# Optimization experiments

Hardware: AMD Instinct MI355X
Metric: run time of the kernel (lower is better)

## Reference

```python
import jax, jax.numpy as jnp
import numpy as np
import math

H = 1024
NH = 16
D = H // NH  # 64
EPS = 1e-5


def _layernorm(x, g, b):
    mu = jnp.mean(x, axis=-1, keepdims=True)
    var = jnp.mean(jnp.square(x - mu), axis=-1, keepdims=True)
    return (x - mu) * jax.lax.rsqrt(var + EPS) * g + b


def setup_inputs() -> dict:
    key = jax.random.key(0)
    ks = jax.random.split(key, 12)
    B, T = 2, 2048
    q = jax.random.normal(ks[0], (B, T, H), jnp.float32)
    k = jax.random.normal(ks[1], (B, T, H), jnp.float32)
    v = jax.random.normal(ks[2], (B, T, H), jnp.float32)
    pad_mask = jax.random.randint(ks[3], (B, T), 0, 2) > 0
    s = 0.02
    Wq = jax.random.normal(ks[4], (H, H), jnp.float32) * s
    Wk = jax.random.normal(ks[5], (H, H), jnp.float32) * s
    Wv = jax.random.normal(ks[6], (H, H), jnp.float32) * s
    Wo = jax.random.normal(ks[7], (H, H), jnp.float32) * s
    W1 = jax.random.normal(ks[8], (4 * H, H), jnp.float32) * s
    b1 = jnp.zeros((4 * H,), jnp.float32)
    W2 = jax.random.normal(ks[9], (H, 4 * H), jnp.float32) * s
    b2 = jnp.zeros((H,), jnp.float32)
    g1 = jnp.ones((H,), jnp.float32); be1 = jnp.zeros((H,), jnp.float32)
    g2 = jnp.ones((H,), jnp.float32); be2 = jnp.zeros((H,), jnp.float32)
    return dict(q=q, k=k, v=v, pad_mask=pad_mask, Wq=Wq, Wk=Wk, Wv=Wv, Wo=Wo,
                W1=W1, b1=b1, W2=W2, b2=b2, g1=g1, be1=be1, g2=g2, be2=be2)


def reference(q, k, v, pad_mask, Wq, Wk, Wv, Wo, W1, b1, W2, b2, g1, be1, g2, be2):
    B, Tq, _ = q.shape
    Tv = v.shape[1]
    # torch nn.Linear: x @ W.T
    Q = (q @ Wq.T).reshape(B, NH, Tq, D)  # faithful to torch .view head split
    K = (k @ Wk.T).reshape(B, NH, Tv, D)
    V = (v @ Wv.T).reshape(B, NH, Tv, D)
    logits = jnp.einsum('baih,bajh->baij', Q, K)  # [B,NH,Tq,Tv]
    neg_inf = jnp.float32(-jnp.inf)
    logits = jnp.where(pad_mask[:, None, None, :], logits, neg_inf)
    attn = jax.nn.softmax(logits / math.sqrt(D), axis=-1)
    # post-softmax query-mask multiply (custom)
    attn = attn * pad_mask[:, None, :, None].astype(attn.dtype)
    h = jnp.einsum('baij,bajh->baih', attn, V).reshape(B, Tq, H)
    h = h @ Wo.T
    h = _layernorm(q + h, g1, be1)
    ff = jax.nn.gelu(h @ W1.T + b1, approximate=False) @ W2.T + b2  # dropout = identity (eval)
    return _layernorm(h + ff, g2, be2)
```

## Files before the change

### kernel.cpp

```cpp
#include <hip/hip_runtime.h>

typedef unsigned short u16;
typedef unsigned int u32;
typedef __attribute__((ext_vector_type(8))) __bf16 bf16x8;
typedef __attribute__((ext_vector_type(4))) float f32x4;
typedef __attribute__((ext_vector_type(16))) float f32x16;
typedef __attribute__((ext_vector_type(4))) unsigned short u16x4;
typedef __attribute__((ext_vector_type(8))) unsigned short u16x8;

#define LOG2E 1.44269504088896340736f

__device__ __forceinline__ u16 f2bf(float f) {
  union { float f; unsigned u; } c; c.f = f;
  unsigned r = c.u + 0x7FFFu + ((c.u >> 16) & 1u);
  return (u16)(r >> 16);
}
__device__ __forceinline__ float bf2f(u16 h) {
  union { unsigned u; float f; } c; c.u = ((unsigned)h) << 16;
  return c.f;
}

__device__ __forceinline__ void gload_lds16(const u16* g, u16* l) {
  __builtin_amdgcn_global_load_lds((const __attribute__((address_space(1))) unsigned int*)g,
                                   (__attribute__((address_space(3))) unsigned int*)l, 16, 0, 0);
}

__device__ __forceinline__ float gelu_fast(float x) {
  float z = fabsf(x) * 0.70710678118654752f;
  float t = 1.0f / (1.0f + 0.3275911f * z);
  float poly = t * (0.254829592f + t * (-0.284496736f + t * (1.421413741f +
               t * (-1.453152027f + t * 1.061405429f))));
  float e = __builtin_amdgcn_exp2f(-z * z * LOG2E);
  float erfz = 1.0f - poly * e;
  float s = (x >= 0.0f) ? erfz : -erfz;
  return 0.5f * x * (1.0f + s);
}

__global__ __launch_bounds__(256) void cvt_all(
    const float* __restrict__ s0, const float* __restrict__ s1, const float* __restrict__ s2,
    const float* __restrict__ s3, const float* __restrict__ s4, const float* __restrict__ s5,
    const float* __restrict__ s6, const float* __restrict__ s7, const float* __restrict__ s8,
    u16* __restrict__ d0, u16* __restrict__ d1, u16* __restrict__ d2,
    u16* __restrict__ d3, u16* __restrict__ d4, u16* __restrict__ d5,
    u16* __restrict__ d6, u16* __restrict__ d7, u16* __restrict__ d8) {
  int i = blockIdx.x * 256 + threadIdx.x;
  if (i >= 6291456) return;
  const float* src; u16* dst; int off;
  if (i < 3145728) {
    if (i < 1048576)      { src = s0; dst = d0; off = 0; }
    else if (i < 2097152) { src = s1; dst = d1; off = 1048576; }
    else                  { src = s2; dst = d2; off = 2097152; }
  } else if (i < 4194304) {
    if (i < 3407872)      { src = s3; dst = d3; off = 3145728; }
    else if (i < 3670016) { src = s4; dst = d4; off = 3407872; }
    else if (i < 3932160) { src = s5; dst = d5; off = 3670016; }
    else                  { src = s6; dst = d6; off = 3932160; }
  } else {
    if (i < 5242880)      { src = s7; dst = d7; off = 4194304; }
    else                  { src = s8; dst = d8; off = 5242880; }
  }
  int j = i - off;
  f32x4 v = ((const f32x4*)src)[j];
  u16x4 o;
  o[0] = f2bf(v[0]); o[1] = f2bf(v[1]); o[2] = f2bf(v[2]); o[3] = f2bf(v[3]);
  ((u16x4*)dst)[j] = o;
}

__global__ void build_masks(const void* __restrict__ pm, float* __restrict__ maskbias,
                            float* __restrict__ qmask, int n) {
  __shared__ int sflag;
  if (threadIdx.x == 0) sflag = 0;
  __syncthreads();
  const unsigned* pw = (const unsigned*)pm;
  int nwords = n / 4;
  int local = 0;
  for (int i = threadIdx.x; i < nwords; i += blockDim.x)
    if (pw[i] > 1u) local = 1;
  if (local) atomicOr(&sflag, 1);
  __syncthreads();
  bool isbool = (sflag != 0);
  for (int i = threadIdx.x; i < n; i += blockDim.x) {
    int m = isbool ? (int)((const unsigned char*)pm)[i] : ((const int*)pm)[i];
    maskbias[i] = m ? 0.0f : -2e30f;
    qmask[i]    = m ? 1.0f : 0.0f;
  }
}

template<int EPI>
__device__ __forceinline__ void gemm_core(const u16* __restrict__ A, const u16* __restrict__ Bw,
                                          const float* __restrict__ bias, u16* __restrict__ C,
                                          int N, int Kstride, int Klen, int bn, int bm, int tid) {
  __shared__ u16 smem[3][8192];
  int wave = tid >> 6, lane = tid & 63;
  int l15 = lane & 15, l4 = lane >> 4;
  int wr = (wave >> 1) * 64, wc = (wave & 1) * 64;
  int mrow0 = bm * 128, ncol0 = bn * 128;
  int srow = lane >> 2;
  int scol = (lane & 3) * 8;

  const u16* asrc0 = A  + (size_t)(mrow0 + (wave * 2 + 0) * 16 + srow) * Kstride + scol;
  const u16* asrc1 = A  + (size_t)(mrow0 + (wave * 2 + 1) * 16 + srow) * Kstride + scol;
  const u16* bsrc0 = Bw + (size_t)(ncol0 + (wave * 2 + 0) * 16 + srow) * Kstride + scol;
  const u16* bsrc1 = Bw + (size_t)(ncol0 + (wave * 2 + 1) * 16 + srow) * Kstride + scol;
  u16* ad0 = &smem[0][(wave * 2 + 0) * 512];
  u16* ad1 = &smem[0][(wave * 2 + 1) * 512];
  u16* bd0 = &smem[0][4096 + (wave * 2 + 0) * 512];
  u16* bd1 = &smem[0][4096 + (wave * 2 + 1) * 512];

  auto stage = [&](int buf, int k0) {
    gload_lds16(asrc0 + k0, ad0 + buf * 8192);
    gload_lds16(asrc1 + k0, ad1 + buf * 8192);
    gload_lds16(bsrc0 + k0, bd0 + buf * 8192);
    gload_lds16(bsrc1 + k0, bd1 + buf * 8192);
  };

  f32x4 acc[4][4];
#pragma unroll
  for (int i = 0; i < 4; i++)
#pragma unroll
    for (int j = 0; j < 4; j++) acc[i][j] = (f32x4)0.0f;

  int nsteps = Klen >> 5;
  stage(0, 0);
  stage(1, 32);
  int cur = 0;
  for (int s = 0; s < nsteps; s++) {
    if (s + 1 < nsteps) {
      asm volatile("s_waitcnt vmcnt(4)" ::: "memory");
    } else {
      asm volatile("s_waitcnt vmcnt(0)" ::: "memory");
    }
    __builtin_amdgcn_s_barrier();
    if (s + 2 < nsteps) {
      int nb = cur + 2; if (nb >= 3) nb -= 3;
      stage(nb, (s + 2) << 5);
    }
    const u16* as = &smem[cur][0];
    const u16* bs = &smem[cur][4096];
    bf16x8 af[4], bfr[4];
#pragma unroll
    for (int mi = 0; mi < 4; mi++) af[mi]  = *(const bf16x8*)(as + (wr + mi * 16 + l15) * 32 + l4 * 8);
#pragma unroll
    for (int ni = 0; ni < 4; ni++) bfr[ni] = *(const bf16x8*)(bs + (wc + ni * 16 + l15) * 32 + l4 * 8);
#pragma unroll
    for (int mi = 0; mi < 4; mi++)
#pragma unroll
      for (int ni = 0; ni < 4; ni++)
        acc[mi][ni] = __builtin_amdgcn_mfma_f32_16x16x32_bf16(af[mi], bfr[ni], acc[mi][ni], 0, 0, 0);
    cur++; if (cur >= 3) cur = 0;
  }

  __syncthreads();
  u16* ct = &smem[0][0];
  for (int p = 0; p < 2; p++) {
    if (p) __syncthreads();
    if ((wave >> 1) == p) {
#pragma unroll
      for (int ni = 0; ni < 4; ni++) {
        int gcol = ncol0 + wc + ni * 16 + l15;
        float bv = (EPI > 0) ? bias[gcol] : 0.0f;
#pragma unroll
        for (int mi = 0; mi < 4; mi++) {
#pragma unroll
          for (int r = 0; r < 4; r++) {
            float v = acc[mi][ni][r] + bv;
            if (EPI == 2) v = gelu_fast(v);
            ct[(mi * 16 + l4 * 4 + r) * 136 + wc + ni * 16 + l15] = f2bf(v);
          }
        }
      }
    }
    __syncthreads();
    int lrow = tid >> 2, cq = tid & 3;
#pragma unroll
    for (int j = 0; j < 4; j++) {
      int col = cq * 8 + j * 32;
      u16x8 vv = *(const u16x8*)(ct + lrow * 136 + col);
      *(u16x8*)(C + (size_t)(mrow0 + p * 64 + lrow) * N + ncol0 + col) = vv;
    }
  }
}

template<int EPI>
__global__ __launch_bounds__(256) void gemm_bt(const u16* __restrict__ A, const u16* __restrict__ Bw,
                                               const float* __restrict__ bias, u16* __restrict__ C,
                                               int N, int K) {
  gemm_core<EPI>(A, Bw, bias, C, N, K, K, blockIdx.x, blockIdx.y, threadIdx.x);
}

__global__ __launch_bounds__(256) void gemm_splitk(const u16* __restrict__ A, const u16* __restrict__ Bw,
                                                   u16* __restrict__ P, int N, int Kstride, int Kc) {
  int z = blockIdx.z;
  size_t M = (size_t)gridDim.y * 128;
  gemm_core<0>(A + (size_t)z * Kc, Bw + (size_t)z * Kc, nullptr,
               P + (size_t)z * M * N, N, Kstride, Kc, blockIdx.x, blockIdx.y, threadIdx.x);
}

__global__ __launch_bounds__(256) void gemm_qkv(const u16* __restrict__ qb, const u16* __restrict__ kb,
                                                const u16* __restrict__ vb,
                                                const u16* __restrict__ wq, const u16* __restrict__ wk,
                                                const u16* __restrict__ wv,
                                                u16* __restrict__ Qo, u16* __restrict__ Ko, u16* __restrict__ Vo) {
  const u16* A; const u16* W; u16* C;
  if (blockIdx.z == 0)      { A = qb; W = wq; C = Qo; }
  else if (blockIdx.z == 1) { A = kb; W = wk; C = Ko; }
  else                      { A = vb; W = wv; C = Vo; }
  gemm_core<0>(A, W, nullptr, C, 1024, 1024, 1024, blockIdx.x, blockIdx.y, threadIdx.x);
}

__global__ __launch_bounds__(256) void transpose64(const u16* __restrict__ in, u16* __restrict__ out) {
  int bh = blockIdx.y, tb = blockIdx.x;
  __shared__ u16 tile[64 * 72];
  int tid = threadIdx.x;
#pragma unroll
  for (int it = 0; it < 2; it++) {
    int idx = it * 256 + tid;
    int r = idx >> 3, c8 = (idx & 7) * 8;
    u16x8 v = *(const u16x8*)(in + ((size_t)bh * 2048 + tb * 64 + r) * 64 + c8);
    int byte = ((r * 72 + c8) * 2) ^ (((r >> 3) & 7) << 4);
    *(u16x8*)((char*)tile + byte) = v;
  }
  __syncthreads();
#pragma unroll
  for (int it = 0; it < 2; it++) {
    int idx = it * 256 + tid;
    int d = idx >> 3, t8 = (idx & 7) * 8;
    u16x8 o;
#pragma unroll
    for (int e = 0; e < 8; e++) {
      int t = t8 + e;
      int byte = ((t * 72 + d) * 2) ^ (((t >> 3) & 7) << 4);
      o[e] = *(const u16*)((const char*)tile + byte);
    }
    *(u16x8*)(out + ((size_t)bh * 64 + d) * 2048 + tb * 64 + t8) = o;
  }
}

__global__ __launch_bounds__(256, 4) void attn4(const u16* __restrict__ Q, const u16* __restrict__ Kg,
                                                const u16* __restrict__ VT,
                                                const float* __restrict__ maskbias,
                                                u16* __restrict__ O0, u16* __restrict__ O1,
                                                float* __restrict__ Ms, float* __restrict__ Ss) {
  const int T = 2048;
  int bh = blockIdx.x;
  int qt = blockIdx.y;
  int sp = blockIdx.z;
  int b = bh >> 4;
  const u16* Qh = Q  + (size_t)bh * T * 64;
  const u16* Kh = Kg + (size_t)bh * T * 64;
  const u16* Vh = VT + (size_t)bh * T * 64;
  u16* Oh = (sp ? O1 : O0) + (size_t)bh * T * 64;
  const float* mb = maskbias + b * T + sp * 1024;
  int tid = threadIdx.x, w = tid >> 6, l = tid & 63;
  int q32 = l & 31, h = l >> 5;
  int qbase = qt * 128 + w * 32;
  const float C = 0.125f * LOG2E;

  __shared__ u16 Ks[2][4096];
  __shared__ u16 Vs[2][4096];

  bf16x8 qf[4];
#pragma unroll
  for (int dc = 0; dc < 4; dc++)
    qf[dc] = *(const bf16x8*)(Qh + (size_t)(qbase + q32) * 64 + dc * 16 + h * 8);

  int rl = l >> 3, ob = (l & 7) * 16;
  int osw = ob ^ (rl << 4);
  int r0 = w * 16 + rl, r1 = w * 16 + 8 + rl;
  const u16* pK0 = Kh + (size_t)(sp * 1024 + r0) * 64 + (osw >> 1);
  const u16* pK1 = Kh + (size_t)(sp * 1024 + r1) * 64 + (osw >> 1);
  const u16* pV0 = Vh + (size_t)r0 * 2048 + sp * 1024 + (osw >> 1);
  const u16* pV1 = Vh + (size_t)r1 * 2048 + sp * 1024 + (osw >> 1);
  u16* dK0 = &Ks[0][0] + (w * 16) * 64;
  u16* dK1 = &Ks[0][0] + (w * 16 + 8) * 64;
  u16* dV0 = &Vs[0][0] + (w * 16) * 64;
  u16* dV1 = &Vs[0][0] + (w * 16 + 8) * 64;

  auto stage = [&](int buf) {
    gload_lds16(pK0, dK0 + buf * 4096);
    gload_lds16(pK1, dK1 + buf * 4096);
    gload_lds16(pV0, dV0 + buf * 4096);
    gload_lds16(pV1, dV1 + buf * 4096);
    pK0 += 4096; pK1 += 4096; pV0 += 64; pV1 += 64;
  };

  f32x16 acc[2];
  acc[0] = (f32x16)0.0f; acc[1] = (f32x16)0.0f;
  float m_ = -3e30f, s_ = 0.0f;

  int swz = (q32 & 7) << 4;

  stage(0);
  for (int t = 0; t < 16; t++) {
    int cur = t & 1;
    __syncthreads();
    if (t < 15) stage(cur ^ 1);
    const char* ksb = (const char*)(&Ks[0][0] + cur * 4096);
    const char* vsb = (const char*)(&Vs[0][0] + cur * 4096);

    bf16x8 kf[2][4];
#pragma unroll
    for (int kvc = 0; kvc < 2; kvc++)
#pragma unroll
      for (int dc = 0; dc < 4; dc++)
        kf[kvc][dc] = *(const bf16x8*)(ksb + (kvc * 32 + q32) * 128 + ((dc * 32 + h * 16) ^ swz));

    f32x16 st[2];
    st[0] = (f32x16)0.0f; st[1] = (f32x16)0.0f;
#pragma unroll
    for (int kvc = 0; kvc < 2; kvc++)
#pragma unroll
      for (int dc = 0; dc < 4; dc++)
        st[kvc] = __builtin_amdgcn_mfma_f32_32x32x16_bf16(kf[kvc][dc], qf[dc], st[kvc], 0, 0, 0);

    float p[32];
    float pmax = -3e30f;
#pragma unroll
    for (int kvc = 0; kvc < 2; kvc++) {
#pragma unroll
      for (int g = 0; g < 4; g++) {
        f32x4 mv = *(const f32x4*)(mb + t * 64 + kvc * 32 + g * 8 + h * 4);
#pragma unroll
        for (int r = 0; r < 4; r++) {
          float val = st[kvc][g * 4 + r] * C + mv[r];
          p[kvc * 16 + g * 4 + r] = val;
          pmax = fmaxf(pmax, val);
        }
      }
    }
    pmax = fmaxf(pmax, __shfl_xor(pmax, 32));

    if (__any(pmax - m_ > 8.0f)) {
      float mnew = fmaxf(m_, pmax);
      float fsc = __builtin_amdgcn_exp2f(m_ - mnew);
      s_ *= fsc;
      m_ = mnew;
#pragma unroll
      for (int g = 0; g < 4; g++)
#pragma unroll
        for (int r = 0; r < 4; r++) {
          float f = __shfl(fsc, g * 8 + h * 4 + r);
          acc[0][g * 4 + r] *= f;
          acc[1][g * 4 + r] *= f;
        }
    }

    float rsum = 0.0f;
    u32 wds[16];
#pragma unroll
    for (int i = 0; i < 16; i++) {
      float a = __builtin_amdgcn_exp2f(p[2 * i] - m_);
      float bq = __builtin_amdgcn_exp2f(p[2 * i + 1] - m_);
      rsum += a + bq;
      union { __bf16 h2[2]; u32 u; } cv;
      cv.h2[0] = (__bf16)a; cv.h2[1] = (__bf16)bq;
      wds[i] = cv.u;
    }
    rsum += __shfl_xor(rsum, 32);
    s_ += rsum;

#pragma unroll
    for (int kvc = 0; kvc < 2; kvc++) {
      int bse = kvc * 8;
      u32 sw0 = __shfl_xor(wds[bse + 0], 32), sw1 = __shfl_xor(wds[bse + 1], 32);
      u32 sw2 = __shfl_xor(wds[bse + 2], 32), sw3 = __shfl_xor(wds[bse + 3], 32);
      u32 sw4 = __shfl_xor(wds[bse + 4], 32), sw5 = __shfl_xor(wds[bse + 5], 32);
      u32 sw6 = __shfl_xor(wds[bse + 6], 32), sw7 = __shfl_xor(wds[bse + 7], 32);
      union { u32 u[4]; bf16x8 v; } pa0, pa1;
      pa0.u[0] = h ? sw2 : wds[bse + 0];
      pa0.u[1] = h ? sw3 : wds[bse + 1];
      pa0.u[2] = h ? wds[bse + 2] : sw0;
      pa0.u[3] = h ? wds[bse + 3] : sw1;
      pa1.u[0] = h ? sw6 : wds[bse + 4];
      pa1.u[1] = h ? sw7 : wds[bse + 5];
      pa1.u[2] = h ? wds[bse + 6] : sw4;
      pa1.u[3] = h ? wds[bse + 7] : sw5;
#pragma unroll
      for (int cl = 0; cl < 2; cl++) {
        bf16x8 pa = cl ? pa1.v : pa0.v;
        int cg = kvc * 2 + cl;
#pragma unroll
        for (int dblk = 0; dblk < 2; dblk++) {
          bf16x8 vf = *(const bf16x8*)(vsb + (dblk * 32 + q32) * 128 + ((cg * 32 + h * 16) ^ swz));
          acc[dblk] = __builtin_amdgcn_mfma_f32_32x32x16_bf16(pa, vf, acc[dblk], 0, 0, 0);
        }
      }
    }
  }

#pragma unroll
  for (int g = 0; g < 4; g++) {
#pragma unroll
    for (int r = 0; r < 4; r++) {
      int row = g * 8 + h * 4 + r;
#pragma unroll
      for (int dblk = 0; dblk < 2; dblk++)
        Oh[(size_t)(qbase + row) * 64 + dblk * 32 + q32] = f2bf(acc[dblk][g * 4 + r]);
    }
  }
  if (h == 0) {
    int ro = sp * 65536 + bh * 2048 + qbase + q32;
    Ms[ro] = m_;
    Ss[ro] = s_;
  }
}

__global__ __launch_bounds__(256) void attn_combine(const u16* __restrict__ O0, const u16* __restrict__ O1,
                                                    const float* __restrict__ Ms, const float* __restrict__ Ss,
                                                    const float* __restrict__ qmaskf, u16* __restrict__ out) {
  int idx = blockIdx.x * 256 + threadIdx.x;
  int row = idx >> 3;
  int d8 = (idx & 7) * 8;
  int bh = row >> 11, r = row & 2047, b = bh >> 4;
  float m0 = Ms[row], m1 = Ms[65536 + row];
  float mstar = fmaxf(m0, m1);
  float w0 = __builtin_amdgcn_exp2f(m0 - mstar);
  float w1 = __builtin_amdgcn_exp2f(m1 - mstar);
  float den = w0 * Ss[row] + w1 * Ss[65536 + row];
  float scale = qmaskf[b * 2048 + r] / den;
  size_t base = (size_t)row * 64 + d8;
  u16x8 a0 = *(const u16x8*)(O0 + base);
  u16x8 a1 = *(const u16x8*)(O1 + base);
  u16x8 o;
#pragma unroll
  for (int e = 0; e < 8; e++)
    o[e] = f2bf((w0 * bf2f(a0[e]) + w1 * bf2f(a1[e])) * scale);
  *(u16x8*)(out + base) = o;
}

template<int NP, int A_F32, int ADD_BIAS, int OUT_F32>
__global__ __launch_bounds__(256) void add_ln_multi(const void* __restrict__ Ap,
                                                    const u16* __restrict__ P0, const u16* __restrict__ P1,
                                                    const u16* __restrict__ P2, const u16* __restrict__ P3,
                                                    const float* __restrict__ bias,
                                                    const float* __restrict__ g, const float* __restrict__ be,
                                                    void* __restrict__ outp) {
  int row = blockIdx.x, tid = threadIdx.x;
  int lane = tid & 63, wave = tid >> 6;
  size_t rb = (size_t)row * 1024;
  float x[4];
  if (A_F32) {
    f32x4 a = ((const f32x4*)((const float*)Ap + rb))[tid];
#pragma unroll
    for (int j = 0; j < 4; j++) x[j] = a[j];
  } else {
    u16x4 au = ((const u16x4*)((const u16*)Ap + rb))[tid];
#pragma unroll
    for (int j = 0; j < 4; j++) x[j] = bf2f(au[j]);
  }
  {
    u16x4 p = ((const u16x4*)(P0 + rb))[tid];
#pragma unroll
    for (int j = 0; j < 4; j++) x[j] += bf2f(p[j]);
  }
  if (NP > 1) {
    u16x4 p = ((const u16x4*)(P1 + rb))[tid];
#pragma unroll
    for (int j = 0; j < 4; j++) x[j] += bf2f(p[j]);
  }
  if (NP > 2) {
    u16x4 p = ((const u16x4*)(P2 + rb))[tid];
#pragma unroll
    for (int j = 0; j < 4; j++) x[j] += bf2f(p[j]);
  }
  if (NP > 3) {
    u16x4 p = ((const u16x4*)(P3 + rb))[tid];
#pragma unroll
    for (int j = 0; j < 4; j++) x[j] += bf2f(p[j]);
  }
  if (ADD_BIAS) {
    f32x4 bv = ((const f32x4*)bias)[tid];
#pragma unroll
    for (int j = 0; j < 4; j++) x[j] += bv[j];
  }
  float s = x[0] + x[1] + x[2] + x[3];
  float q = x[0] * x[0] + x[1] * x[1] + x[2] * x[2] + x[3] * x[3];
#pragma unroll
  for (int m = 1; m < 64; m <<= 1) { s += __shfl_xor(s, m); q += __shfl_xor(q, m); }
  __shared__ float rs[4], rq[4];
  if (lane == 0) { rs[wave] = s; rq[wave] = q; }
  __syncthreads();
  float S = rs[0] + rs[1] + rs[2] + rs[3];
  float Qq = rq[0] + rq[1] + rq[2] + rq[3];
  float mean = S * (1.0f / 1024.0f);
  float var = Qq * (1.0f / 1024.0f) - mean * mean;
  float rstd = rsqrtf(var + 1e-5f);
  if (OUT_F32) {
    f32x4 y;
#pragma unroll
    for (int j = 0; j < 4; j++) { int col = tid * 4 + j; y[j] = (x[j] - mean) * rstd * g[col] + be[col]; }
    ((f32x4*)((float*)outp + rb))[tid] = y;
  } else {
    u16x4 y;
#pragma unroll
    for (int j = 0; j < 4; j++) { int col = tid * 4 + j; y[j] = f2bf((x[j] - mean) * rstd * g[col] + be[col]); }
    ((u16x4*)((u16*)outp + rb))[tid] = y;
  }
}

extern "C" void kernel_launch(void* const* d_in, const int* in_sizes, int n_in,
                              void* d_out, int out_size, void* d_ws, size_t ws_size,
                              hipStream_t stream) {
  const float* q   = (const float*)d_in[0];
  const float* k   = (const float*)d_in[1];
  const float* v   = (const float*)d_in[2];
  const void*  pad = d_in[3];
  const float* Wq  = (const float*)d_in[4];
  const float* Wk  = (const float*)d_in[5];
  const float* Wv  = (const float*)d_in[6];
  const float* Wo  = (const float*)d_in[7];
  const float* W1  = (const float*)d_in[8];
  const float* b1  = (const float*)d_in[9];
  const float* W2  = (const float*)d_in[10];
  const float* b2  = (const float*)d_in[11];
  const float* g1  = (const float*)d_in[12];
  const float* be1 = (const float*)d_in[13];
  const float* g2  = (const float*)d_in[14];
  const float* be2 = (const float*)d_in[15];
  float* out = (float*)d_out;
  char* ws = (char*)d_ws;
  const size_t MB = 1u << 20;

  u16* wq_b = (u16*)(ws + 0 * MB);
  u16* wk_b = (u16*)(ws + 2 * MB);
  u16* wv_b = (u16*)(ws + 4 * MB);
  u16* wo_b = (u16*)(ws + 6 * MB);
  u16* w1_b = (u16*)(ws + 8 * MB);
  u16* w2_b = (u16*)(ws + 16 * MB);
  u16* qb   = (u16*)(ws + 24 * MB);
  u16* kb   = (u16*)(ws + 32 * MB);
  u16* vb   = (u16*)(ws + 40 * MB);
  u16* Qb   = (u16*)(ws + 48 * MB);
  u16* Kb   = (u16*)(ws + 56 * MB);
  u16* Vb   = (u16*)(ws + 64 * MB);
  u16* VTb  = (u16*)(ws + 72 * MB);
  u16* hatt = (u16*)(ws + 80 * MB);
  u16* Op0  = (u16*)(ws + 24 * MB);
  u16* Op1  = (u16*)(ws + 32 * MB);
  float* Ms = (float*)(ws + 88 * MB);
  float* Ss = (float*)(ws + 89 * MB);
  u16* WP   = (u16*)(ws + 40 * MB);
  u16* h1b  = (u16*)(ws + 24 * MB);
  u16* ff1  = (u16*)(ws + 32 * MB);
  u16* Fp   = (u16*)(ws + 64 * MB);
  float* maskbias = (float*)(ws + 96 * MB);
  float* qmaskf   = (float*)(ws + 96 * MB + 16384);

  build_masks<<<1, 256, 0, stream>>>(pad, maskbias, qmaskf, in_sizes[3]);

  cvt_all<<<24576, 256, 0, stream>>>(q, k, v, Wq, Wk, Wv, Wo, W1, W2,
                                     qb, kb, vb, wq_b, wk_b, wv_b, wo_b, w1_b, w2_b);

  gemm_qkv<<<dim3(8, 32, 3), 256, 0, stream>>>(qb, kb, vb, wq_b, wk_b, wv_b, Qb, Kb, Vb);

  transpose64<<<dim3(32, 32), 256, 0, stream>>>(Vb, VTb);

  attn4<<<dim3(32, 16, 2), 256, 0, stream>>>(Qb, Kb, VTb, maskbias, Op0, Op1, Ms, Ss);

  attn_combine<<<2048, 256, 0, stream>>>(Op0, Op1, Ms, Ss, qmaskf, hatt);

  gemm_splitk<<<dim3(8, 32, 2), 256, 0, stream>>>(hatt, wo_b, WP, 1024, 1024, 512);

  add_ln_multi<2, 1, 0, 0><<<4096, 256, 0, stream>>>(q, WP, WP + 4194304, nullptr, nullptr,
                                                     nullptr, g1, be1, h1b);

  gemm_bt<2><<<dim3(32, 32), 256, 0, stream>>>(h1b, w1_b, b1, ff1, 4096, 1024);

  gemm_splitk<<<dim3(8, 32, 4), 256, 0, stream>>>(ff1, w2_b, Fp, 1024, 4096, 1024);

  add_ln_multi<4, 0, 1, 1><<<4096, 256, 0, stream>>>(h1b, Fp, Fp + 4194304, Fp + 2 * 4194304,
                                                     Fp + 3 * 4194304, b2, g2, be2, out);
}
```

Measured before the change: 302.7 us.

## Use 8 waves per GEMM tile with smaller per-wave subtiles

After: 279.1 us. 1.08x faster.

```diff
diff --git a/kernel.cpp b/kernel.cpp
--- a/kernel.cpp
+++ b/kernel.cpp
@@ -93,30 +93,25 @@
   __shared__ u16 smem[3][8192];
   int wave = tid >> 6, lane = tid & 63;
   int l15 = lane & 15, l4 = lane >> 4;
-  int wr = (wave >> 1) * 64, wc = (wave & 1) * 64;
+  int wr = (wave >> 1) * 32;
+  int wc = (wave & 1) * 64;
   int mrow0 = bm * 128, ncol0 = bn * 128;
   int srow = lane >> 2;
   int scol = (lane & 3) * 8;
 
-  const u16* asrc0 = A  + (size_t)(mrow0 + (wave * 2 + 0) * 16 + srow) * Kstride + scol;
-  const u16* asrc1 = A  + (size_t)(mrow0 + (wave * 2 + 1) * 16 + srow) * Kstride + scol;
-  const u16* bsrc0 = Bw + (size_t)(ncol0 + (wave * 2 + 0) * 16 + srow) * Kstride + scol;
-  const u16* bsrc1 = Bw + (size_t)(ncol0 + (wave * 2 + 1) * 16 + srow) * Kstride + scol;
-  u16* ad0 = &smem[0][(wave * 2 + 0) * 512];
-  u16* ad1 = &smem[0][(wave * 2 + 1) * 512];
-  u16* bd0 = &smem[0][4096 + (wave * 2 + 0) * 512];
-  u16* bd1 = &smem[0][4096 + (wave * 2 + 1) * 512];
+  const u16* asrc = A  + (size_t)(mrow0 + wave * 16 + srow) * Kstride + scol;
+  const u16* bsrc = Bw + (size_t)(ncol0 + wave * 16 + srow) * Kstride + scol;
+  u16* ad = &smem[0][wave * 512];
+  u16* bd = &smem[0][4096 + wave * 512];
 
   auto stage = [&](int buf, int k0) {
-    gload_lds16(asrc0 + k0, ad0 + buf * 8192);
-    gload_lds16(asrc1 + k0, ad1 + buf * 8192);
-    gload_lds16(bsrc0 + k0, bd0 + buf * 8192);
-    gload_lds16(bsrc1 + k0, bd1 + buf * 8192);
+    gload_lds16(asrc + k0, ad + buf * 8192);
+    gload_lds16(bsrc + k0, bd + buf * 8192);
   };
 
-  f32x4 acc[4][4];
-#pragma unroll
-  for (int i = 0; i < 4; i++)
+  f32x4 acc[2][4];
+#pragma unroll
+  for (int i = 0; i < 2; i++)
 #pragma unroll
     for (int j = 0; j < 4; j++) acc[i][j] = (f32x4)0.0f;
 
@@ -126,7 +121,7 @@
   int cur = 0;
   for (int s = 0; s < nsteps; s++) {
     if (s + 1 < nsteps) {
-      asm volatile("s_waitcnt vmcnt(4)" ::: "memory");
+      asm volatile("s_waitcnt vmcnt(2)" ::: "memory");
     } else {
       asm volatile("s_waitcnt vmcnt(0)" ::: "memory");
     }
@@ -137,13 +132,13 @@
     }
     const u16* as = &smem[cur][0];
     const u16* bs = &smem[cur][4096];
-    bf16x8 af[4], bfr[4];
-#pragma unroll
-    for (int mi = 0; mi < 4; mi++) af[mi]  = *(const bf16x8*)(as + (wr + mi * 16 + l15) * 32 + l4 * 8);
+    bf16x8 af[2], bfr[4];
+#pragma unroll
+    for (int mi = 0; mi < 2; mi++) af[mi]  = *(const bf16x8*)(as + (wr + mi * 16 + l15) * 32 + l4 * 8);
 #pragma unroll
     for (int ni = 0; ni < 4; ni++) bfr[ni] = *(const bf16x8*)(bs + (wc + ni * 16 + l15) * 32 + l4 * 8);
 #pragma unroll
-    for (int mi = 0; mi < 4; mi++)
+    for (int mi = 0; mi < 2; mi++)
 #pragma unroll
       for (int ni = 0; ni < 4; ni++)
         acc[mi][ni] = __builtin_amdgcn_mfma_f32_16x16x32_bf16(af[mi], bfr[ni], acc[mi][ni], 0, 0, 0);
@@ -152,55 +147,50 @@
 
   __syncthreads();
   u16* ct = &smem[0][0];
-  for (int p = 0; p < 2; p++) {
-    if (p) __syncthreads();
-    if ((wave >> 1) == p) {
-#pragma unroll
-      for (int ni = 0; ni < 4; ni++) {
-        int gcol = ncol0 + wc + ni * 16 + l15;
-        float bv = (EPI > 0) ? bias[gcol] : 0.0f;
-#pragma unroll
-        for (int mi = 0; mi < 4; mi++) {
-#pragma unroll
-          for (int r = 0; r < 4; r++) {
-            float v = acc[mi][ni][r] + bv;
-            if (EPI == 2) v = gelu_fast(v);
-            ct[(mi * 16 + l4 * 4 + r) * 136 + wc + ni * 16 + l15] = f2bf(v);
-          }
-        }
+#pragma unroll
+  for (int ni = 0; ni < 4; ni++) {
+    int gcol = ncol0 + wc + ni * 16 + l15;
+    float bv = (EPI > 0) ? bias[gcol] : 0.0f;
+#pragma unroll
+    for (int mi = 0; mi < 2; mi++) {
+#pragma unroll
+      for (int r = 0; r < 4; r++) {
+        float v = acc[mi][ni][r] + bv;
+        if (EPI == 2) v = gelu_fast(v);
+        ct[(wr + mi * 16 + l4 * 4 + r) * 136 + wc + ni * 16 + l15] = f2bf(v);
       }
     }
-    __syncthreads();
-    int lrow = tid >> 2, cq = tid & 3;
-#pragma unroll
-    for (int j = 0; j < 4; j++) {
-      int col = cq * 8 + j * 32;
-      u16x8 vv = *(const u16x8*)(ct + lrow * 136 + col);
-      *(u16x8*)(C + (size_t)(mrow0 + p * 64 + lrow) * N + ncol0 + col) = vv;
-    }
+  }
+  __syncthreads();
+  int lrow = tid >> 2, cq = tid & 3;
+#pragma unroll
+  for (int j = 0; j < 4; j++) {
+    int col = cq * 8 + j * 32;
+    u16x8 vv = *(const u16x8*)(ct + lrow * 136 + col);
+    *(u16x8*)(C + (size_t)(mrow0 + lrow) * N + ncol0 + col) = vv;
   }
 }
 
 template<int EPI>
-__global__ __launch_bounds__(256) void gemm_bt(const u16* __restrict__ A, const u16* __restrict__ Bw,
-                                               const float* __restrict__ bias, u16* __restrict__ C,
-                                               int N, int K) {
+__global__ __launch_bounds__(512, 4) void gemm_bt(const u16* __restrict__ A, const u16* __restrict__ Bw,
+                                                  const float* __restrict__ bias, u16* __restrict__ C,
+                                                  int N, int K) {
   gemm_core<EPI>(A, Bw, bias, C, N, K, K, blockIdx.x, blockIdx.y, threadIdx.x);
 }
 
-__global__ __launch_bounds__(256) void gemm_splitk(const u16* __restrict__ A, const u16* __restrict__ Bw,
-                                                   u16* __restrict__ P, int N, int Kstride, int Kc) {
+__global__ __launch_bounds__(512, 4) void gemm_splitk(const u16* __restrict__ A, const u16* __restrict__ Bw,
+                                                      u16* __restrict__ P, int N, int Kstride, int Kc) {
   int z = blockIdx.z;
   size_t M = (size_t)gridDim.y * 128;
   gemm_core<0>(A + (size_t)z * Kc, Bw + (size_t)z * Kc, nullptr,
                P + (size_t)z * M * N, N, Kstride, Kc, blockIdx.x, blockIdx.y, threadIdx.x);
 }
 
-__global__ __launch_bounds__(256) void gemm_qkv(const u16* __restrict__ qb, const u16* __restrict__ kb,
-                                                const u16* __restrict__ vb,
-                                                const u16* __restrict__ wq, const u16* __restrict__ wk,
-                                                const u16* __restrict__ wv,
-                                                u16* __restrict__ Qo, u16* __restrict__ Ko, u16* __restrict__ Vo) {
+__global__ __launch_bounds__(512, 4) void gemm_qkv(const u16* __restrict__ qb, const u16* __restrict__ kb,
+                                                   const u16* __restrict__ vb,
+                                                   const u16* __restrict__ wq, const u16* __restrict__ wk,
+                                                   const u16* __restrict__ wv,
+                                                   u16* __restrict__ Qo, u16* __restrict__ Ko, u16* __restrict__ Vo) {
   const u16* A; const u16* W; u16* C;
   if (blockIdx.z == 0)      { A = qb; W = wq; C = Qo; }
   else if (blockIdx.z == 1) { A = kb; W = wk; C = Ko; }
@@ -551,7 +541,7 @@
   cvt_all<<<24576, 256, 0, stream>>>(q, k, v, Wq, Wk, Wv, Wo, W1, W2,
                                      qb, kb, vb, wq_b, wk_b, wv_b, wo_b, w1_b, w2_b);
 
-  gemm_qkv<<<dim3(8, 32, 3), 256, 0, stream>>>(qb, kb, vb, wq_b, wk_b, wv_b, Qb, Kb, Vb);
+  gemm_qkv<<<dim3(8, 32, 3), 512, 0, stream>>>(qb, kb, vb, wq_b, wk_b, wv_b, Qb, Kb, Vb);
 
   transpose64<<<dim3(32, 32), 256, 0, stream>>>(Vb, VTb);
 
@@ -559,14 +549,14 @@
 
   attn_combine<<<2048, 256, 0, stream>>>(Op0, Op1, Ms, Ss, qmaskf, hatt);
 
-  gemm_splitk<<<dim3(8, 32, 2), 256, 0, stream>>>(hatt, wo_b, WP, 1024, 1024, 512);
+  gemm_splitk<<<dim3(8, 32, 2), 512, 0, stream>>>(hatt, wo_b, WP, 1024, 1024, 512);
 
   add_ln_multi<2, 1, 0, 0><<<4096, 256, 0, stream>>>(q, WP, WP + 4194304, nullptr, nullptr,
                                                      nullptr, g1, be1, h1b);
 
-  gemm_bt<2><<<dim3(32, 32), 256, 0, stream>>>(h1b, w1_b, b1, ff1, 4096, 1024);
-
-  gemm_splitk<<<dim3(8, 32, 4), 256, 0, stream>>>(ff1, w2_b, Fp, 1024, 4096, 1024);
+  gemm_bt<2><<<dim3(32, 32), 512, 0, stream>>>(h1b, w1_b, b1, ff1, 4096, 1024);
+
+  gemm_splitk<<<dim3(8, 32, 4), 512, 0, stream>>>(ff1, w2_b, Fp, 1024, 4096, 1024);
 
   add_ln_multi<4, 0, 1, 1><<<4096, 256, 0, stream>>>(h1b, Fp, Fp + 4194304, Fp + 2 * 4194304,
                                                      Fp + 3 * 4194304, b2, g2, be2, out);
```
